# Performance work log

Measured on AMD Instinct MI355X. Metric: run time of the kernel, lower is better.

The kernel has to match this reference:

```python
import jax, jax.numpy as jnp
import numpy as np

LEFT, RIGHT = 64, 64  # left_size, right_size; hidden = LEFT*RIGHT = 4096


def _cayley(raw):
    """torch nn.utils.parametrizations.orthogonal(..., orthogonal_map='cayley',
    use_trivialization=False): A = triu(raw, 1); X = A - A^T (skew-symmetric);
    Q = (I - X/2)^{-1} (I + X/2)."""
    n = raw.shape[0]
    A = jnp.triu(raw, 1)
    X = A - A.T
    Id = jnp.eye(n, dtype=raw.dtype)
    return jnp.linalg.solve(Id - 0.5 * X, Id + 0.5 * X)


def setup_inputs() -> dict:
    key = jax.random.key(0)
    ks = jax.random.split(key, 8)
    B, S = 4, 2048
    H = LEFT * RIGHT
    inp = jax.random.normal(ks[0], (B, S, H), dtype=jnp.float32)
    raw_u_left = jax.random.normal(ks[1], (LEFT, LEFT), dtype=jnp.float32) * 0.02
    raw_v_left = jax.random.normal(ks[2], (LEFT, LEFT), dtype=jnp.float32) * 0.02
    raw_u_right = jax.random.normal(ks[3], (RIGHT, RIGHT), dtype=jnp.float32) * 0.02
    raw_v_right = jax.random.normal(ks[4], (RIGHT, RIGHT), dtype=jnp.float32) * 0.02
    diag_left = jnp.ones((LEFT,), dtype=jnp.float32)
    diag_right = jnp.ones((RIGHT,), dtype=jnp.float32)
    diag_scale = jnp.ones((H,), dtype=jnp.float32) + 0.01 * jax.random.normal(ks[5], (H,), dtype=jnp.float32)
    return {
        "inp": inp,
        "raw_u_left": raw_u_left,
        "raw_v_left": raw_v_left,
        "diag_left": diag_left,
        "raw_u_right": raw_u_right,
        "raw_v_right": raw_v_right,
        "diag_right": diag_right,
        "diag_scale": diag_scale,
        "inv_t": 0,
    }


def reference(inp, raw_u_left, raw_v_left, diag_left, raw_u_right, raw_v_right,
              diag_right, diag_scale, inv_t):
    # add_diag=True, use_diag=True path
    if inv_t:
        x = inp / diag_scale
        dl = 1.0 / diag_left
        dr = 1.0 / diag_right
    else:
        x = inp * diag_scale
        dl = diag_left
        dr = diag_right
    # Cayley-parametrized orthogonal factors
    Ul = _cayley(raw_u_left)
    Vl = _cayley(raw_v_left)
    Ur = _cayley(raw_u_right)
    Vr = _cayley(raw_v_right)
    # SVD-style reconstruction: M = U @ diag(d) @ V^T
    ML = (Ul * dl[None, :]) @ Vl.T  # [LEFT, LEFT]
    MR = (Ur * dr[None, :]) @ Vr.T  # [RIGHT, RIGHT]
    # Kronecker matmul: view last dim as [LEFT, RIGHT], out = ML^T @ X @ MR
    orig_shape = x.shape
    xb = x.reshape(-1, LEFT, RIGHT)  # [B*S, LEFT, RIGHT]
    out = jnp.einsum('bij,ik,jl->bkl', xb, ML, MR)
    return out.reshape(orig_shape)
```

## Files before the change

kernel.cpp:

```cpp
#include <hip/hip_runtime.h>
#include <hip/hip_bf16.h>

typedef short short8 __attribute__((ext_vector_type(8)));
typedef float f32x4 __attribute__((ext_vector_type(4)));
typedef float f32x16 __attribute__((ext_vector_type(16)));
typedef unsigned int u32x4 __attribute__((ext_vector_type(4)));

#define HID 4096
#define CST 68

#define LGKM0 do { asm volatile("s_waitcnt lgkmcnt(0)" ::: "memory"); \
                   __builtin_amdgcn_sched_barrier(0); } while (0)

__device__ __forceinline__ unsigned short f2bf(float f) {
    unsigned int u = __float_as_uint(f);
    u = (u + 0x7FFFu + ((u >> 16) & 1u)) >> 16;
    return (unsigned short)u;
}

__device__ __forceinline__ f32x4 mm4(const float* SA, const float* SB, int i, int j0) {
    f32x4 acc = {0.f, 0.f, 0.f, 0.f};
#pragma unroll 8
    for (int k = 0; k < 64; ++k) {
        float a = SA[i * CST + k];
        acc += a * *reinterpret_cast<const f32x4*>(SB + k * CST + j0);
    }
    return acc;
}

__global__ __launch_bounds__(1024) void cayley_build_kernel(
    const float* __restrict__ rul, const float* __restrict__ rvl, const float* __restrict__ dl,
    const float* __restrict__ rur, const float* __restrict__ rvr, const float* __restrict__ dr,
    const int* __restrict__ invt,
    unsigned short* __restrict__ plp, unsigned short* __restrict__ mrp)
{
    __shared__ __align__(16) float Yw[64 * CST], Aw[64 * CST], Pw[64 * CST];
    __shared__ __align__(16) float Qw[64 * CST], QTw[64 * CST];
    __shared__ float dd[64];

    const float* ru; const float* rv; const float* dv; unsigned short* ob;
    if (blockIdx.x == 0) { ru = rul; rv = rvl; dv = dl; ob = plp; }
    else                 { ru = rur; rv = rvr; dv = dr; ob = mrp; }

    const int tid = threadIdx.x;
    const int i = tid >> 4;
    const int j0 = (tid & 15) << 2;

    for (int pass = 0; pass < 2; ++pass) {
        const float* raw = (pass == 0) ? ru : rv;
#pragma unroll
        for (int q = 0; q < 4; ++q) {
            int j = j0 + q;
            float v = 0.f;
            if (j > i)      v =  raw[i * 64 + j];
            else if (j < i) v = -raw[j * 64 + i];
            Yw[i * CST + j] = 0.5f * v;
        }
        __syncthreads();
        f32x4 a = mm4(Yw, Yw, i, j0);
        __syncthreads();
        *reinterpret_cast<f32x4*>(Aw + i * CST + j0) = a;
        *reinterpret_cast<f32x4*>(Pw + i * CST + j0) =
            a + *reinterpret_cast<const f32x4*>(Yw + i * CST + j0);
        __syncthreads();
        a = mm4(Pw, Aw, i, j0);
        __syncthreads();
        *reinterpret_cast<f32x4*>(Pw + i * CST + j0) += a;
        __syncthreads();
        a = mm4(Aw, Aw, i, j0);
        __syncthreads();
        *reinterpret_cast<f32x4*>(Aw + i * CST + j0) = a;
        __syncthreads();
        a = mm4(Pw, Aw, i, j0);
        __syncthreads();
        f32x4 p = *reinterpret_cast<const f32x4*>(Pw + i * CST + j0) + a;
#pragma unroll
        for (int q = 0; q < 4; ++q) {
            int j = j0 + q;
            float qv = ((i == j) ? 1.f : 0.f) + 2.f * p[q];
            if (pass == 0) Qw[i * CST + j]  = qv;
            else           QTw[j * CST + i] = qv;
        }
        __syncthreads();
    }
    if (tid < 64) { float d = dv[tid]; dd[tid] = (invt[0] != 0) ? (1.0f / d) : d; }
    __syncthreads();

    f32x4 m = {0.f, 0.f, 0.f, 0.f};
#pragma unroll 8
    for (int j = 0; j < 64; ++j) {
        float aa = Qw[i * CST + j] * dd[j];
        m += aa * *reinterpret_cast<const f32x4*>(QTw + j * CST + j0);
    }
    const int kt = i >> 4, hh = (i >> 3) & 1, e = i & 7;
#pragma unroll
    for (int q = 0; q < 4; ++q) {
        int j = j0 + q;
        unsigned short v = f2bf(m[q]);
        int dst;
        if (blockIdx.x == 0)
            dst = (((j >> 5) * 4 + kt) * 64 + (j & 31) + 32 * hh) * 8 + e;
        else
            dst = ((kt * 2 + (j >> 5)) * 64 + (j & 31) + 32 * hh) * 8 + e;
        ob[dst] = v;
    }
}

__global__ __launch_bounds__(256, 4) void kron_kernel(
    const float* __restrict__ inp, const float* __restrict__ ds,
    const unsigned short* __restrict__ plp, const unsigned short* __restrict__ mrp,
    const int* __restrict__ invt, float* __restrict__ out, int ntok)
{
    __shared__ __align__(16) unsigned char sbuf[4][8192];
    const int w = threadIdx.x >> 6;
    const int lane = threadIdx.x & 63;
    const int r = lane & 31;
    const int h = lane >> 5;
    unsigned char* S = sbuf[w];

    const int t = blockIdx.x * 4 + w;
    if (t >= ntok) return;
    const bool inv = (invt[0] != 0);
    const float* xt = inp + (size_t)t * HID;

#pragma unroll
    for (int s = 0; s < 8; ++s) {
        const int fi = s * 512 + lane * 8;
        f32x4 x0 = *reinterpret_cast<const f32x4*>(xt + fi);
        f32x4 x1 = *reinterpret_cast<const f32x4*>(xt + fi + 4);
        f32x4 d0 = *reinterpret_cast<const f32x4*>(ds + fi);
        f32x4 d1 = *reinterpret_cast<const f32x4*>(ds + fi + 4);
        if (inv) {
#pragma unroll
            for (int e = 0; e < 4; ++e) { x0[e] /= d0[e]; x1[e] /= d1[e]; }
        } else {
            x0 *= d0; x1 *= d1;
        }
        short8 f;
#pragma unroll
        for (int e = 0; e < 4; ++e) {
            f[e]     = (short)f2bf(x0[e]);
            f[e + 4] = (short)f2bf(x1[e]);
        }
        const int m = s * 8 + (lane >> 3);
        const int c = lane & 7;
        *reinterpret_cast<short8*>(S + ((m * 8 + (c ^ (m & 7))) << 4)) = f;
    }
    LGKM0;

    unsigned int zs[4][8];
#pragma unroll
    for (int nt = 0; nt < 2; ++nt) {
        short8 b1[4];
#pragma unroll
        for (int kt = 0; kt < 4; ++kt)
            b1[kt] = *reinterpret_cast<const short8*>(
                mrp + ((kt * 2 + nt) * 64 + lane) * 8);
#pragma unroll
        for (int mt = 0; mt < 2; ++mt) {
            short8 a1[4];
#pragma unroll
            for (int kt = 0; kt < 4; ++kt)
                a1[kt] = *reinterpret_cast<const short8*>(
                    S + (((32 * mt + r) * 8 + ((2 * kt + h) ^ (r & 7))) << 4));
            f32x16 acc = {0.f};
#pragma unroll
            for (int kt = 0; kt < 4; ++kt)
                acc = __builtin_amdgcn_mfma_f32_32x32x16_bf16(a1[kt], b1[kt], acc, 0, 0, 0);
            unsigned int q[8];
#pragma unroll
            for (int p = 0; p < 8; ++p)
                q[p] = (unsigned int)f2bf(acc[2 * p]) |
                       ((unsigned int)f2bf(acc[2 * p + 1]) << 16);
            auto s02 = __builtin_amdgcn_permlane32_swap(q[0], q[2], false, false);
            auto s13 = __builtin_amdgcn_permlane32_swap(q[1], q[3], false, false);
            auto s46 = __builtin_amdgcn_permlane32_swap(q[4], q[6], false, false);
            auto s57 = __builtin_amdgcn_permlane32_swap(q[5], q[7], false, false);
            unsigned int* z = zs[mt * 2 + nt];
            z[0] = s02[0]; z[1] = s13[0]; z[2] = s02[1]; z[3] = s13[1];
            z[4] = s46[0]; z[5] = s57[0]; z[6] = s46[1]; z[7] = s57[1];
        }
    }
    LGKM0;

    float* Lf = reinterpret_cast<float*>(S);
    float* op = out + (size_t)t * HID;
#pragma unroll
    for (int mt2 = 0; mt2 < 2; ++mt2) {
        short8 a2[4];
#pragma unroll
        for (int kt = 0; kt < 4; ++kt)
            a2[kt] = *reinterpret_cast<const short8*>(
                plp + ((mt2 * 4 + kt) * 64 + lane) * 8);
#pragma unroll
        for (int nt2 = 0; nt2 < 2; ++nt2) {
            f32x16 y = {0.f};
#pragma unroll
            for (int kt2 = 0; kt2 < 4; ++kt2) {
                const unsigned int* z = zs[(kt2 >> 1) * 2 + nt2];
                const int kb = (kt2 & 1) * 4;
                union { u32x4 u; short8 s; } cv;
                cv.u[0] = z[kb + 0]; cv.u[1] = z[kb + 1];
                cv.u[2] = z[kb + 2]; cv.u[3] = z[kb + 3];
                y = __builtin_amdgcn_mfma_f32_32x32x16_bf16(a2[kt2], cv.s, y, 0, 0, 0);
            }
#pragma unroll
            for (int g = 0; g < 16; ++g) {
                const int kk = (g & 3) + 8 * (g >> 2) + 4 * h;
                const int c  = 32 * nt2 + r;
                Lf[(kk * 16 + ((c >> 2) ^ (kk & 15))) * 4 + (c & 3)] = y[g];
            }
        }
        LGKM0;
#pragma unroll
        for (int s = 0; s < 8; ++s) {
            const int f  = s * 64 + lane;
            const int kk = f >> 4;
            const int cg = f & 15;
            f32x4 v = *reinterpret_cast<const f32x4*>(
                Lf + (kk * 16 + (cg ^ (kk & 15))) * 4);
            *reinterpret_cast<f32x4*>(op + (32 * mt2 + kk) * 64 + cg * 4) = v;
        }
        LGKM0;
    }
}

extern "C" void kernel_launch(void* const* d_in, const int* in_sizes, int n_in,
                              void* d_out, int out_size, void* d_ws, size_t ws_size,
                              hipStream_t stream) {
    const float* inp = (const float*)d_in[0];
    const float* rul = (const float*)d_in[1];
    const float* rvl = (const float*)d_in[2];
    const float* dl  = (const float*)d_in[3];
    const float* rur = (const float*)d_in[4];
    const float* rvr = (const float*)d_in[5];
    const float* dr  = (const float*)d_in[6];
    const float* ds  = (const float*)d_in[7];
    const int*   invt = (const int*)d_in[8];
    float* out = (float*)d_out;

    unsigned short* plp = (unsigned short*)d_ws;
    unsigned short* mrp = plp + 4096;

    const int ntok = in_sizes[0] / HID;

    hipLaunchKernelGGL(cayley_build_kernel, dim3(2), dim3(1024), 0, stream,
                       rul, rvl, dl, rur, rvr, dr, invt, plp, mrp);
    const int nblk = (ntok + 3) / 4;
    hipLaunchKernelGGL(kron_kernel, dim3(nblk), dim3(256), 0, stream,
                       inp, ds, plp, mrp, invt, out, ntok);
}
```

Before: 83.93 us.

## Process multiple tokens per wave with register prefetch and cached scale/weights

Each wave now handles four tokens in sequence instead of one. The MFMA weight fragments for both factor matrices are loaded into registers once per wave. The diag_scale vector, already inverted when inv_t is set, is staged in shared memory once per block, and the next token's input is prefetched into registers while the current one is processed. This removes redundant weight and scale loads and overlaps global reads with compute, in exchange for higher register and LDS use, launch bounds lowered to 2, and fewer blocks (512).

Result: slower. 90.77 us (+8.1%).

```diff
diff --git a/kernel.cpp b/kernel.cpp
--- a/kernel.cpp
+++ b/kernel.cpp
@@ -8,6 +8,7 @@
 
 #define HID 4096
 #define CST 68
+#define TPW 4
 
 #define LGKM0 do { asm volatile("s_waitcnt lgkmcnt(0)" ::: "memory"); \
                    __builtin_amdgcn_sched_barrier(0); } while (0)
@@ -106,122 +107,153 @@
     }
 }
 
-__global__ __launch_bounds__(256, 4) void kron_kernel(
+__global__ __launch_bounds__(256, 2) void kron_kernel(
     const float* __restrict__ inp, const float* __restrict__ ds,
     const unsigned short* __restrict__ plp, const unsigned short* __restrict__ mrp,
     const int* __restrict__ invt, float* __restrict__ out, int ntok)
 {
     __shared__ __align__(16) unsigned char sbuf[4][8192];
+    __shared__ __align__(16) float dsb[4096];
     const int w = threadIdx.x >> 6;
     const int lane = threadIdx.x & 63;
     const int r = lane & 31;
     const int h = lane >> 5;
     unsigned char* S = sbuf[w];
-
-    const int t = blockIdx.x * 4 + w;
-    if (t >= ntok) return;
     const bool inv = (invt[0] != 0);
-    const float* xt = inp + (size_t)t * HID;
-
-#pragma unroll
-    for (int s = 0; s < 8; ++s) {
-        const int fi = s * 512 + lane * 8;
-        f32x4 x0 = *reinterpret_cast<const f32x4*>(xt + fi);
-        f32x4 x1 = *reinterpret_cast<const f32x4*>(xt + fi + 4);
-        f32x4 d0 = *reinterpret_cast<const f32x4*>(ds + fi);
-        f32x4 d1 = *reinterpret_cast<const f32x4*>(ds + fi + 4);
+
+    for (int i = threadIdx.x; i < 1024; i += 256) {
+        f32x4 d = *reinterpret_cast<const f32x4*>(ds + i * 4);
         if (inv) {
 #pragma unroll
-            for (int e = 0; e < 4; ++e) { x0[e] /= d0[e]; x1[e] /= d1[e]; }
-        } else {
-            x0 *= d0; x1 *= d1;
-        }
-        short8 f;
-#pragma unroll
-        for (int e = 0; e < 4; ++e) {
-            f[e]     = (short)f2bf(x0[e]);
-            f[e + 4] = (short)f2bf(x1[e]);
-        }
-        const int m = s * 8 + (lane >> 3);
-        const int c = lane & 7;
-        *reinterpret_cast<short8*>(S + ((m * 8 + (c ^ (m & 7))) << 4)) = f;
-    }
-    LGKM0;
-
-    unsigned int zs[4][8];
-#pragma unroll
-    for (int nt = 0; nt < 2; ++nt) {
-        short8 b1[4];
+            for (int e = 0; e < 4; ++e) d[e] = 1.0f / d[e];
+        }
+        *reinterpret_cast<f32x4*>(dsb + i * 4) = d;
+    }
+
+    short8 b1[8], a2[8];
+#pragma unroll
+    for (int kt = 0; kt < 4; ++kt)
+#pragma unroll
+        for (int nt = 0; nt < 2; ++nt)
+            b1[kt * 2 + nt] = *reinterpret_cast<const short8*>(
+                mrp + ((kt * 2 + nt) * 64 + lane) * 8);
+#pragma unroll
+    for (int mt = 0; mt < 2; ++mt)
 #pragma unroll
         for (int kt = 0; kt < 4; ++kt)
-            b1[kt] = *reinterpret_cast<const short8*>(
-                mrp + ((kt * 2 + nt) * 64 + lane) * 8);
-#pragma unroll
-        for (int mt = 0; mt < 2; ++mt) {
-            short8 a1[4];
-#pragma unroll
-            for (int kt = 0; kt < 4; ++kt)
-                a1[kt] = *reinterpret_cast<const short8*>(
-                    S + (((32 * mt + r) * 8 + ((2 * kt + h) ^ (r & 7))) << 4));
-            f32x16 acc = {0.f};
-#pragma unroll
-            for (int kt = 0; kt < 4; ++kt)
-                acc = __builtin_amdgcn_mfma_f32_32x32x16_bf16(a1[kt], b1[kt], acc, 0, 0, 0);
-            unsigned int q[8];
-#pragma unroll
-            for (int p = 0; p < 8; ++p)
-                q[p] = (unsigned int)f2bf(acc[2 * p]) |
-                       ((unsigned int)f2bf(acc[2 * p + 1]) << 16);
-            auto s02 = __builtin_amdgcn_permlane32_swap(q[0], q[2], false, false);
-            auto s13 = __builtin_amdgcn_permlane32_swap(q[1], q[3], false, false);
-            auto s46 = __builtin_amdgcn_permlane32_swap(q[4], q[6], false, false);
-            auto s57 = __builtin_amdgcn_permlane32_swap(q[5], q[7], false, false);
-            unsigned int* z = zs[mt * 2 + nt];
-            z[0] = s02[0]; z[1] = s13[0]; z[2] = s02[1]; z[3] = s13[1];
-            z[4] = s46[0]; z[5] = s57[0]; z[6] = s46[1]; z[7] = s57[1];
-        }
-    }
-    LGKM0;
-
-    float* Lf = reinterpret_cast<float*>(S);
-    float* op = out + (size_t)t * HID;
-#pragma unroll
-    for (int mt2 = 0; mt2 < 2; ++mt2) {
-        short8 a2[4];
-#pragma unroll
-        for (int kt = 0; kt < 4; ++kt)
-            a2[kt] = *reinterpret_cast<const short8*>(
-                plp + ((mt2 * 4 + kt) * 64 + lane) * 8);
-#pragma unroll
-        for (int nt2 = 0; nt2 < 2; ++nt2) {
-            f32x16 y = {0.f};
-#pragma unroll
-            for (int kt2 = 0; kt2 < 4; ++kt2) {
-                const unsigned int* z = zs[(kt2 >> 1) * 2 + nt2];
-                const int kb = (kt2 & 1) * 4;
-                union { u32x4 u; short8 s; } cv;
-                cv.u[0] = z[kb + 0]; cv.u[1] = z[kb + 1];
-                cv.u[2] = z[kb + 2]; cv.u[3] = z[kb + 3];
-                y = __builtin_amdgcn_mfma_f32_32x32x16_bf16(a2[kt2], cv.s, y, 0, 0, 0);
-            }
-#pragma unroll
-            for (int g = 0; g < 16; ++g) {
-                const int kk = (g & 3) + 8 * (g >> 2) + 4 * h;
-                const int c  = 32 * nt2 + r;
-                Lf[(kk * 16 + ((c >> 2) ^ (kk & 15))) * 4 + (c & 3)] = y[g];
+            a2[mt * 4 + kt] = *reinterpret_cast<const short8*>(
+                plp + ((mt * 4 + kt) * 64 + lane) * 8);
+    __syncthreads();
+
+    const int t0 = (blockIdx.x * 4 + w) * TPW;
+    if (t0 >= ntok) return;
+
+    f32x4 xb[16];
+    {
+        const float* xt = inp + (size_t)t0 * HID;
+#pragma unroll
+        for (int s = 0; s < 8; ++s) {
+            xb[2 * s]     = *reinterpret_cast<const f32x4*>(xt + s * 512 + lane * 8);
+            xb[2 * s + 1] = *reinterpret_cast<const f32x4*>(xt + s * 512 + lane * 8 + 4);
+        }
+    }
+
+    for (int it = 0; it < TPW; ++it) {
+        const int t = t0 + it;
+        if (t >= ntok) break;
+
+#pragma unroll
+        for (int s = 0; s < 8; ++s) {
+            f32x4 d0 = *reinterpret_cast<const f32x4*>(dsb + s * 512 + lane * 8);
+            f32x4 d1 = *reinterpret_cast<const f32x4*>(dsb + s * 512 + lane * 8 + 4);
+            f32x4 x0 = xb[2 * s] * d0;
+            f32x4 x1 = xb[2 * s + 1] * d1;
+            short8 f;
+#pragma unroll
+            for (int e = 0; e < 4; ++e) {
+                f[e]     = (short)f2bf(x0[e]);
+                f[e + 4] = (short)f2bf(x1[e]);
+            }
+            const int m = s * 8 + (lane >> 3);
+            const int c = lane & 7;
+            *reinterpret_cast<short8*>(S + ((m * 8 + (c ^ (m & 7))) << 4)) = f;
+        }
+
+        if (it + 1 < TPW && t + 1 < ntok) {
+            const float* xt = inp + (size_t)(t + 1) * HID;
+#pragma unroll
+            for (int s = 0; s < 8; ++s) {
+                xb[2 * s]     = *reinterpret_cast<const f32x4*>(xt + s * 512 + lane * 8);
+                xb[2 * s + 1] = *reinterpret_cast<const f32x4*>(xt + s * 512 + lane * 8 + 4);
             }
         }
         LGKM0;
-#pragma unroll
-        for (int s = 0; s < 8; ++s) {
-            const int f  = s * 64 + lane;
-            const int kk = f >> 4;
-            const int cg = f & 15;
-            f32x4 v = *reinterpret_cast<const f32x4*>(
-                Lf + (kk * 16 + (cg ^ (kk & 15))) * 4);
-            *reinterpret_cast<f32x4*>(op + (32 * mt2 + kk) * 64 + cg * 4) = v;
+
+        unsigned int zs[4][8];
+#pragma unroll
+        for (int nt = 0; nt < 2; ++nt) {
+#pragma unroll
+            for (int mt = 0; mt < 2; ++mt) {
+                short8 a1[4];
+#pragma unroll
+                for (int kt = 0; kt < 4; ++kt)
+                    a1[kt] = *reinterpret_cast<const short8*>(
+                        S + (((32 * mt + r) * 8 + ((2 * kt + h) ^ (r & 7))) << 4));
+                f32x16 acc = {0.f};
+#pragma unroll
+                for (int kt = 0; kt < 4; ++kt)
+                    acc = __builtin_amdgcn_mfma_f32_32x32x16_bf16(a1[kt], b1[kt * 2 + nt], acc, 0, 0, 0);
+                unsigned int q[8];
+#pragma unroll
+                for (int p = 0; p < 8; ++p)
+                    q[p] = (unsigned int)f2bf(acc[2 * p]) |
+                           ((unsigned int)f2bf(acc[2 * p + 1]) << 16);
+                auto s02 = __builtin_amdgcn_permlane32_swap(q[0], q[2], false, false);
+                auto s13 = __builtin_amdgcn_permlane32_swap(q[1], q[3], false, false);
+                auto s46 = __builtin_amdgcn_permlane32_swap(q[4], q[6], false, false);
+                auto s57 = __builtin_amdgcn_permlane32_swap(q[5], q[7], false, false);
+                unsigned int* z = zs[mt * 2 + nt];
+                z[0] = s02[0]; z[1] = s13[0]; z[2] = s02[1]; z[3] = s13[1];
+                z[4] = s46[0]; z[5] = s57[0]; z[6] = s46[1]; z[7] = s57[1];
+            }
         }
         LGKM0;
+
+        float* Lf = reinterpret_cast<float*>(S);
+        float* op = out + (size_t)t * HID;
+#pragma unroll
+        for (int mt2 = 0; mt2 < 2; ++mt2) {
+#pragma unroll
+            for (int nt2 = 0; nt2 < 2; ++nt2) {
+                f32x16 y = {0.f};
+#pragma unroll
+                for (int kt2 = 0; kt2 < 4; ++kt2) {
+                    const unsigned int* z = zs[(kt2 >> 1) * 2 + nt2];
+                    const int kb = (kt2 & 1) * 4;
+                    union { u32x4 u; short8 s; } cv;
+                    cv.u[0] = z[kb + 0]; cv.u[1] = z[kb + 1];
+                    cv.u[2] = z[kb + 2]; cv.u[3] = z[kb + 3];
+                    y = __builtin_amdgcn_mfma_f32_32x32x16_bf16(a2[mt2 * 4 + kt2], cv.s, y, 0, 0, 0);
+                }
+#pragma unroll
+                for (int g = 0; g < 16; ++g) {
+                    const int kk = (g & 3) + 8 * (g >> 2) + 4 * h;
+                    const int c  = 32 * nt2 + r;
+                    Lf[(kk * 16 + ((c >> 2) ^ (kk & 15))) * 4 + (c & 3)] = y[g];
+                }
+            }
+            LGKM0;
+#pragma unroll
+            for (int s = 0; s < 8; ++s) {
+                const int f  = s * 64 + lane;
+                const int kk = f >> 4;
+                const int cg = f & 15;
+                f32x4 v = *reinterpret_cast<const f32x4*>(
+                    Lf + (kk * 16 + (cg ^ (kk & 15))) * 4);
+                *reinterpret_cast<f32x4*>(op + (32 * mt2 + kk) * 64 + cg * 4) = v;
+            }
+            LGKM0;
+        }
     }
 }
 
@@ -246,7 +278,8 @@
 
     hipLaunchKernelGGL(cayley_build_kernel, dim3(2), dim3(1024), 0, stream,
                        rul, rvl, dl, rur, rvr, dr, invt, plp, mrp);
-    const int nblk = (ntok + 3) / 4;
+    const int tpb = 4 * TPW;
+    const int nblk = (ntok + tpb - 1) / tpb;
     hipLaunchKernelGGL(kron_kernel, dim3(nblk), dim3(256), 0, stream,
                        inp, ds, plp, mrp, invt, out, ntok);
 }
```
